# Performance work log

Measured on AMD Instinct MI355X. Metric: run time of the kernel, lower is better.

## Reference

```python
import jax, jax.numpy as jnp
import numpy as np

P_MINUS_1 = 1.0      # p=2 -> (p-1)
LCP_BETA = 32.0
LOG_ALPHA = float(np.log(2.0))  # alpha=2.0
KDIG = 8
N_HEAD = 16


def _rope(x, cos, sin):
    # x: (B,T,H,D), cos/sin: (T,D//2)
    d = x.shape[-1] // 2
    x1, x2 = x[..., :d], x[..., d:]
    c = cos[None, :, None, :]
    s = sin[None, :, None, :]
    return jnp.concatenate([x1 * c - x2 * s, x1 * s + x2 * c], axis=-1)


def _rms_norm(x, eps=1e-6):
    return x * jax.lax.rsqrt(jnp.mean(jnp.square(x), axis=-1, keepdims=True) + eps)


def setup_inputs() -> dict:
    key = jax.random.key(0)
    ks = jax.random.split(key, 9)
    B, T, C, H = 2, 512, 1024, N_HEAD
    D = C // H
    std = 0.02
    x = jax.random.normal(ks[0], (B, T, C), jnp.float32)
    cos = jax.random.uniform(ks[1], (T, D // 2), jnp.float32)
    sin = jax.random.uniform(ks[2], (T, D // 2), jnp.float32)
    Wq = jax.random.normal(ks[3], (C, C), jnp.float32) * std
    Wk = jax.random.normal(ks[4], (C, C), jnp.float32) * std
    Wv = jax.random.normal(ks[5], (C, C), jnp.float32) * std
    Wo = jax.random.normal(ks[6], (C, C), jnp.float32) * std
    # to_digits_* use flax default lecun_normal: std = 1/sqrt(fan_in)
    Wdq = jax.random.normal(ks[7], (D, KDIG), jnp.float32) / np.sqrt(D)
    Wdk = jax.random.normal(ks[8], (D, KDIG), jnp.float32) / np.sqrt(D)
    return {"x": x, "cos": cos, "sin": sin, "Wq": Wq, "Wk": Wk, "Wv": Wv,
            "Wo": Wo, "Wdq": Wdq, "Wdk": Wdk}


def _soft_lcp_depth(q_digits, k_digits):
    # q_digits: (B,H,Tq,K), k_digits: (B,H,Tk,K) -> (B,H,Tq,Tk)
    diff = jnp.abs(q_digits[:, :, :, None, :] - k_digits[:, :, None, :, :])
    match_prob = jnp.exp(-LCP_BETA * jnp.square(diff))
    prefix_prob = jnp.cumprod(match_prob, axis=-1)
    return jnp.sum(prefix_prob, axis=-1)


def reference(x, cos, sin, Wq, Wk, Wv, Wo, Wdq, Wdk):
    B, T, C = x.shape
    H = N_HEAD
    D = C // H
    q = (x @ Wq).reshape(B, T, H, D)
    k = (x @ Wk).reshape(B, T, H, D)
    v = (x @ Wv).reshape(B, T, H, D)
    q = _rms_norm(_rope(q, cos, sin))
    k = _rms_norm(_rope(k, cos, sin))
    q = jnp.transpose(q, (0, 2, 1, 3))  # (B,H,T,D)
    k = jnp.transpose(k, (0, 2, 1, 3))
    v = jnp.transpose(v, (0, 2, 1, 3))
    # causal keep mask (T,T), broadcast over (B,H)
    keep = jnp.tril(jnp.ones((T, T), dtype=bool))[None, None]
    q_digits = jax.nn.sigmoid((q @ Wdq).astype(jnp.float32)) * P_MINUS_1
    k_digits = jax.nn.sigmoid((k @ Wdk).astype(jnp.float32)) * P_MINUS_1
    lcp = _soft_lcp_depth(q_digits, k_digits)  # (B,H,T,T)
    weights = jnp.exp(lcp * LOG_ALPHA)
    weights = jnp.where(keep, weights, 0.0)
    denom = jnp.maximum(jnp.sum(weights, axis=-1, keepdims=True), 1e-9)
    attn = weights / denom
    y = jnp.einsum('bhqk,bhkd->bhqd', attn.astype(v.dtype), v)
    y = jnp.transpose(y, (0, 2, 1, 3)).reshape(B, T, C)
    return y @ Wo
```

## Files before the change

### kernel.cpp

```cpp
#include <hip/hip_runtime.h>

#define T_SEQ 512
#define CDIM  1024
#define NH    16
#define DH    64
#define BB    2
#define KD    8

#define BETA_LOG2E 46.16624131f
#define LOG2E      1.4426950408889634f

typedef unsigned short u16;
typedef __attribute__((ext_vector_type(8))) short bf16x8;
typedef __attribute__((ext_vector_type(4))) float f32x4;

__device__ inline u16 f2bf(float f) {
    unsigned int u = __builtin_bit_cast(unsigned int, f);
    unsigned int r = (u + 0x7fffu + ((u >> 16) & 1u)) >> 16;
    return (u16)r;
}
__device__ inline float bf2f(u16 v) {
    unsigned int u = ((unsigned int)v) << 16;
    return __builtin_bit_cast(float, u);
}

__device__ inline void gload_lds16(const void* g, void* l) {
    __builtin_amdgcn_global_load_lds(
        (const __attribute__((address_space(1))) void*)g,
        (__attribute__((address_space(3))) void*)l, 16, 0, 0);
}

__global__ __launch_bounds__(256)
void prep_kernel(const float* __restrict__ x,
                 const float* __restrict__ W0, const float* __restrict__ W1,
                 const float* __restrict__ W2, const float* __restrict__ W3,
                 u16* __restrict__ xb,
                 u16* __restrict__ T0, u16* __restrict__ T1,
                 u16* __restrict__ T2, u16* __restrict__ T3)
{
    const int tid = threadIdx.x;
    if (blockIdx.z == 4) {
        const int row = blockIdx.y * 32 + (tid >> 3);
        const int col = blockIdx.x * 32 + (tid & 7) * 4;
        float4 v = *(const float4*)&x[(size_t)row * CDIM + col];
        ushort4 o = { f2bf(v.x), f2bf(v.y), f2bf(v.z), f2bf(v.w) };
        *(ushort4*)&xb[(size_t)row * CDIM + col] = o;
        return;
    }
    __shared__ u16 tile[32][33];
    const float* W = (blockIdx.z == 0) ? W0 : (blockIdx.z == 1) ? W1
                   : (blockIdx.z == 2) ? W2 : W3;
    u16* Tt        = (blockIdx.z == 0) ? T0 : (blockIdx.z == 1) ? T1
                   : (blockIdx.z == 2) ? T2 : T3;
    const int k0 = blockIdx.y * 32, n0 = blockIdx.x * 32;
    const int r = tid >> 3, c4 = (tid & 7) * 4;

    float4 v = *(const float4*)&W[(size_t)(k0 + r) * CDIM + n0 + c4];
    tile[r][c4 + 0] = f2bf(v.x);
    tile[r][c4 + 1] = f2bf(v.y);
    tile[r][c4 + 2] = f2bf(v.z);
    tile[r][c4 + 3] = f2bf(v.w);
    __syncthreads();
    ushort4 o;
    o.x = tile[c4 + 0][r];
    o.y = tile[c4 + 1][r];
    o.z = tile[c4 + 2][r];
    o.w = tile[c4 + 3][r];
    *(ushort4*)&Tt[(size_t)(n0 + r) * CDIM + k0 + c4] = o;
}

__global__ __launch_bounds__(256)
void gemm_qkv_fused(const u16* __restrict__ A,
                    const u16* __restrict__ Bq, const u16* __restrict__ Bk,
                    const u16* __restrict__ Bv,
                    const float* __restrict__ cosp, const float* __restrict__ sinp,
                    const float* __restrict__ Wdq, const float* __restrict__ Wdk,
                    float* __restrict__ qdig, float* __restrict__ kdig,
                    u16* __restrict__ Vt)
{
    __shared__ __align__(16) char smem[64 * 65 * 4];
    u16* As = (u16*)smem;
    u16* Bs = As + 4096;
    float* Cf = (float*)smem;

    const int z = blockIdx.z;
    const u16* Bt = (z == 0) ? Bq : (z == 1) ? Bk : Bv;

    const int tid = threadIdx.x;
    const int l = tid & 63, w = tid >> 6;
    const int m0 = blockIdx.y * 64;
    const int h  = blockIdx.x;
    const int n0 = h * 64;
    const int wr = (w >> 1) * 32, wc = (w & 1) * 32;

    const int srow = l >> 3;
    const int sslot = (l & 7) ^ srow;

    f32x4 acc[2][2];
    #pragma unroll
    for (int i = 0; i < 2; ++i)
        #pragma unroll
        for (int j = 0; j < 2; ++j)
            acc[i][j] = (f32x4){0.f, 0.f, 0.f, 0.f};

    for (int k0 = 0; k0 < CDIM; k0 += 64) {
        __syncthreads();
        #pragma unroll
        for (int q = 0; q < 2; ++q) {
            const int row = w * 16 + q * 8 + srow;
            gload_lds16(A  + (size_t)(m0 + row) * CDIM + k0 + sslot * 8,
                        &As[(w * 16 + q * 8) * 64]);
            gload_lds16(Bt + (size_t)(n0 + row) * CDIM + k0 + sslot * 8,
                        &Bs[(w * 16 + q * 8) * 64]);
        }
        __syncthreads();

        bf16x8 af[2][2], bfr[2][2];
        #pragma unroll
        for (int i = 0; i < 2; ++i)
            #pragma unroll
            for (int kh = 0; kh < 2; ++kh) {
                const int ra = wr + i * 16 + (l & 15);
                const int sa = (kh * 4 + (l >> 4)) ^ (ra & 7);
                af[i][kh] = *(const bf16x8*)&As[ra * 64 + sa * 8];
                const int rb = wc + i * 16 + (l & 15);
                const int sb = (kh * 4 + (l >> 4)) ^ (rb & 7);
                bfr[i][kh] = *(const bf16x8*)&Bs[rb * 64 + sb * 8];
            }
        #pragma unroll
        for (int kh = 0; kh < 2; ++kh)
            #pragma unroll
            for (int i = 0; i < 2; ++i)
                #pragma unroll
                for (int j = 0; j < 2; ++j)
                    acc[i][j] = __builtin_amdgcn_mfma_f32_16x16x32_bf16(
                        af[i][kh], bfr[j][kh], acc[i][j], 0, 0, 0);
    }

    __syncthreads();

    if (z == 2) {
        #pragma unroll
        for (int i = 0; i < 2; ++i)
            #pragma unroll
            for (int j = 0; j < 2; ++j) {
                const int mm = wr + i * 16 + (l >> 4) * 4;
                const int dd = wc + j * 16 + (l & 15);
                #pragma unroll
                for (int r = 0; r < 4; ++r)
                    Cf[dd * 65 + mm + r] = acc[i][j][r];
            }
        __syncthreads();
        const int b = m0 >> 9, t0 = m0 & (T_SEQ - 1);
        u16* vbase = Vt + ((size_t)(b * NH + h) * 64) * T_SEQ;
        #pragma unroll
        for (int it = 0; it < 16; ++it) {
            const int d = it * 4 + w;
            vbase[(size_t)d * T_SEQ + t0 + l] = f2bf(Cf[d * 65 + l]);
        }
        return;
    }

    #pragma unroll
    for (int i = 0; i < 2; ++i)
        #pragma unroll
        for (int j = 0; j < 2; ++j) {
            const int mm = wr + i * 16 + (l >> 4) * 4;
            const int dd = wc + j * 16 + (l & 15);
            #pragma unroll
            for (int r = 0; r < 4; ++r)
                Cf[(mm + r) * 65 + dd] = acc[i][j][r];
        }

    const float* Wd = z ? Wdk : Wdq;
    float* dig = z ? kdig : qdig;

    const int dl = l & 15, rq = l >> 4;
    float wreg[4][8];
    #pragma unroll
    for (int d4 = 0; d4 < 4; ++d4) {
        *(float4*)&wreg[d4][0] = *(const float4*)&Wd[(dl + d4 * 16) * 8];
        *(float4*)&wreg[d4][4] = *(const float4*)&Wd[(dl + d4 * 16) * 8 + 4];
    }
    __syncthreads();

    for (int g = 0; g < 4; ++g) {
        const int m = w * 16 + g * 4 + rq;
        const int mg = m0 + m;
        const int b = mg >> 9, t = mg & (T_SEQ - 1);

        const float* cr = &Cf[m * 65];
        float r0 = cr[dl], r1 = cr[dl + 16], r2 = cr[dl + 32], r3 = cr[dl + 48];
        float c0 = cosp[t * 32 + dl], c1 = cosp[t * 32 + dl + 16];
        float s0 = sinp[t * 32 + dl], s1 = sinp[t * 32 + dl + 16];
        float v0 = r0 * c0 - r2 * s0;
        float v1 = r1 * c1 - r3 * s1;
        float v2 = r0 * s0 + r2 * c0;
        float v3 = r1 * s1 + r3 * c1;

        float ss = v0 * v0 + v1 * v1 + v2 * v2 + v3 * v3;
        #pragma unroll
        for (int off = 1; off < 16; off <<= 1) ss += __shfl_xor(ss, off);
        float sc = rsqrtf(ss * (1.0f / 64.0f) + 1e-6f);
        v0 *= sc; v1 *= sc; v2 *= sc; v3 *= sc;

        float zz[8];
        #pragma unroll
        for (int j = 0; j < 8; ++j)
            zz[j] = v0 * wreg[0][j] + v1 * wreg[1][j] + v2 * wreg[2][j] + v3 * wreg[3][j];
        #pragma unroll
        for (int j = 0; j < 8; ++j) {
            #pragma unroll
            for (int off = 1; off < 16; off <<= 1) zz[j] += __shfl_xor(zz[j], off);
        }
        float zsel = zz[0];
        #pragma unroll
        for (int j = 1; j < 8; ++j) zsel = (dl == j) ? zz[j] : zsel;
        if (dl < 8)
            dig[((size_t)(b * NH + h) * T_SEQ + t) * KD + dl] =
                1.0f / (1.0f + exp2f(-LOG2E * zsel));
    }
}

__global__ __launch_bounds__(256)
void attn_partial(const float* __restrict__ qdig, const float* __restrict__ kdig,
                  const u16* __restrict__ Vt,
                  u16* __restrict__ pacc, float* __restrict__ pdeng)
{
    __shared__ u16 Vs[4096];
    __shared__ u16 Ps[4096];
    __shared__ float qds[512];

    const int tid = threadIdx.x;
    const int w = tid >> 6, l = tid & 63;
    const int h = blockIdx.y, b = blockIdx.z;
    const int bh = b * NH + h;
    const size_t bhT = (size_t)bh * T_SEQ;

    int id = blockIdx.x, c = 0;
    while (id >= c + 1) { id -= (c + 1); ++c; }
    const int kt = id;
    const int k0 = kt * 64;

    const int srow = l >> 3, sslot = (l & 7) ^ srow;
    #pragma unroll
    for (int q2 = 0; q2 < 2; ++q2) {
        const int R0 = w * 16 + q2 * 8;
        gload_lds16(Vt + ((size_t)bh * 64 + R0 + srow) * T_SEQ + k0 + sslot * 8,
                    &Vs[R0 * 64]);
    }
    *(float2*)&qds[tid * 2] = *(const float2*)&qdig[(bhT + c * 64) * KD + tid * 2];

    float kd[8];
    {
        const float* kp = &kdig[(bhT + k0 + l) * KD];
        *(float4*)&kd[0] = *(const float4*)kp;
        *(float4*)&kd[4] = *(const float4*)(kp + 4);
    }
    __syncthreads();

    const bool diag = (kt == c);
    for (int qi = 0; qi < 16; ++qi) {
        const int qrow = w * 16 + qi;
        float qd[8];
        *(float4*)&qd[0] = *(const float4*)&qds[qrow * 8];
        *(float4*)&qd[4] = *(const float4*)&qds[qrow * 8 + 4];
        float cum = 1.f, lcp = 0.f;
        #pragma unroll
        for (int jj = 0; jj < 8; ++jj) {
            float d = qd[jj] - kd[jj];
            cum *= exp2f(-BETA_LOG2E * d * d);
            lcp += cum;
        }
        float wgt = exp2f(lcp);
        if (diag && l > qrow) wgt = 0.f;
        Ps[qrow * 64 + (((l >> 3) ^ (qi & 7)) << 3) + (l & 7)] = f2bf(wgt);
    }
    __syncthreads();

    const int wr = (w >> 1) * 32, wc = (w & 1) * 32;
    f32x4 acc[2][2], accd[2];
    #pragma unroll
    for (int i = 0; i < 2; ++i) {
        accd[i] = (f32x4){0.f, 0.f, 0.f, 0.f};
        #pragma unroll
        for (int j = 0; j < 2; ++j) acc[i][j] = (f32x4){0.f, 0.f, 0.f, 0.f};
    }
    bf16x8 ones;
    #pragma unroll
    for (int i = 0; i < 8; ++i) ones[i] = (short)0x3F80;

    #pragma unroll
    for (int kh = 0; kh < 2; ++kh) {
        bf16x8 af[2], bfr[2];
        #pragma unroll
        for (int i = 0; i < 2; ++i) {
            const int ra = wr + i * 16 + (l & 15);
            const int sa = (kh * 4 + (l >> 4)) ^ (ra & 7);
            af[i] = *(const bf16x8*)&Ps[ra * 64 + sa * 8];
            const int rb = wc + i * 16 + (l & 15);
            const int sb = (kh * 4 + (l >> 4)) ^ (rb & 7);
            bfr[i] = *(const bf16x8*)&Vs[rb * 64 + sb * 8];
        }
        #pragma unroll
        for (int i = 0; i < 2; ++i) {
            accd[i] = __builtin_amdgcn_mfma_f32_16x16x32_bf16(af[i], ones, accd[i], 0, 0, 0);
            #pragma unroll
            for (int j = 0; j < 2; ++j)
                acc[i][j] = __builtin_amdgcn_mfma_f32_16x16x32_bf16(
                    af[i], bfr[j], acc[i][j], 0, 0, 0);
        }
    }

    const int task = bh * 36 + blockIdx.x;
    u16* pa = pacc + (size_t)task * 4096;
    #pragma unroll
    for (int i = 0; i < 2; ++i) {
        const int row = wr + i * 16 + (l >> 4) * 4;
        #pragma unroll
        for (int j = 0; j < 2; ++j) {
            const int col = wc + j * 16 + (l & 15);
            #pragma unroll
            for (int r = 0; r < 4; ++r)
                pa[(size_t)(row + r) * 64 + col] = f2bf(acc[i][j][r]);
        }
        if ((l & 15) == 0) {
            #pragma unroll
            for (int r = 0; r < 4; ++r)
                pdeng[(size_t)task * 64 + row + r] = accd[i][r];
        }
    }
}

__global__ __launch_bounds__(256)
void attn_combine(const u16* __restrict__ pacc, const float* __restrict__ pdeng,
                  u16* __restrict__ y)
{
    const int c = blockIdx.x, h = blockIdx.y, b = blockIdx.z;
    const int tid = threadIdx.x;
    const int r = tid >> 2, dg = (tid & 3) * 16;
    const int base = (b * NH + h) * 36 + c * (c + 1) / 2;

    float acc[16] = {};
    float den = 0.f;
    for (int kt = 0; kt <= c; ++kt) {
        const u16* pa = pacc + (size_t)(base + kt) * 4096 + r * 64 + dg;
        ushort4 v0 = *(const ushort4*)(pa + 0);
        ushort4 v1 = *(const ushort4*)(pa + 4);
        ushort4 v2 = *(const ushort4*)(pa + 8);
        ushort4 v3 = *(const ushort4*)(pa + 12);
        acc[0]  += bf2f(v0.x); acc[1]  += bf2f(v0.y);
        acc[2]  += bf2f(v0.z); acc[3]  += bf2f(v0.w);
        acc[4]  += bf2f(v1.x); acc[5]  += bf2f(v1.y);
        acc[6]  += bf2f(v1.z); acc[7]  += bf2f(v1.w);
        acc[8]  += bf2f(v2.x); acc[9]  += bf2f(v2.y);
        acc[10] += bf2f(v2.z); acc[11] += bf2f(v2.w);
        acc[12] += bf2f(v3.x); acc[13] += bf2f(v3.y);
        acc[14] += bf2f(v3.z); acc[15] += bf2f(v3.w);
        den += pdeng[(size_t)(base + kt) * 64 + r];
    }
    float inv = 1.f / fmaxf(den, 1e-9f);

    u16* yr = y + ((size_t)(b * T_SEQ + c * 64 + r)) * CDIM + h * DH + dg;
    uint4 p0, p1;
    p0.x = f2bf(acc[0] * inv)  | ((unsigned)f2bf(acc[1] * inv)  << 16);
    p0.y = f2bf(acc[2] * inv)  | ((unsigned)f2bf(acc[3] * inv)  << 16);
    p0.z = f2bf(acc[4] * inv)  | ((unsigned)f2bf(acc[5] * inv)  << 16);
    p0.w = f2bf(acc[6] * inv)  | ((unsigned)f2bf(acc[7] * inv)  << 16);
    p1.x = f2bf(acc[8] * inv)  | ((unsigned)f2bf(acc[9] * inv)  << 16);
    p1.y = f2bf(acc[10] * inv) | ((unsigned)f2bf(acc[11] * inv) << 16);
    p1.z = f2bf(acc[12] * inv) | ((unsigned)f2bf(acc[13] * inv) << 16);
    p1.w = f2bf(acc[14] * inv) | ((unsigned)f2bf(acc[15] * inv) << 16);
    *(uint4*)(yr + 0) = p0;
    *(uint4*)(yr + 8) = p1;
}

__global__ __launch_bounds__(256)
void gemm_proj(const u16* __restrict__ A, const u16* __restrict__ Bt,
               float* __restrict__ C)
{
    __shared__ u16 As[32 * 64];
    __shared__ u16 Bs[64 * 64];

    const int tid = threadIdx.x;
    const int l = tid & 63, w = tid >> 6;
    const int m0 = blockIdx.y * 32, n0 = blockIdx.x * 64;
    const int wr = (w & 1) * 16, wc = (w >> 1) * 32;
    const int srow = l >> 3;
    const int sslot = (l & 7) ^ srow;

    f32x4 acc[2];
    acc[0] = (f32x4){0.f, 0.f, 0.f, 0.f};
    acc[1] = (f32x4){0.f, 0.f, 0.f, 0.f};

    for (int k0 = 0; k0 < CDIM; k0 += 64) {
        __syncthreads();
        {
            const int rowa = w * 8 + srow;
            gload_lds16(A + (size_t)(m0 + rowa) * CDIM + k0 + sslot * 8,
                        &As[(w * 8) * 64]);
        }
        #pragma unroll
        for (int q = 0; q < 2; ++q) {
            const int row = w * 16 + q * 8 + srow;
            gload_lds16(Bt + (size_t)(n0 + row) * CDIM + k0 + sslot * 8,
                        &Bs[(w * 16 + q * 8) * 64]);
        }
        __syncthreads();

        bf16x8 af[2], bfr[2][2];
        #pragma unroll
        for (int kh = 0; kh < 2; ++kh) {
            const int ra = wr + (l & 15);
            const int sa = (kh * 4 + (l >> 4)) ^ (ra & 7);
            af[kh] = *(const bf16x8*)&As[ra * 64 + sa * 8];
            #pragma unroll
            for (int j = 0; j < 2; ++j) {
                const int rb = wc + j * 16 + (l & 15);
                const int sb = (kh * 4 + (l >> 4)) ^ (rb & 7);
                bfr[j][kh] = *(const bf16x8*)&Bs[rb * 64 + sb * 8];
            }
        }
        #pragma unroll
        for (int kh = 0; kh < 2; ++kh)
            #pragma unroll
            for (int j = 0; j < 2; ++j)
                acc[j] = __builtin_amdgcn_mfma_f32_16x16x32_bf16(
                    af[kh], bfr[j][kh], acc[j], 0, 0, 0);
    }

    #pragma unroll
    for (int j = 0; j < 2; ++j) {
        const int row = m0 + wr + (l >> 4) * 4;
        const int col = n0 + wc + j * 16 + (l & 15);
        #pragma unroll
        for (int r = 0; r < 4; ++r)
            C[(size_t)(row + r) * CDIM + col] = acc[j][r];
    }
}

extern "C" void kernel_launch(void* const* d_in, const int* in_sizes, int n_in,
                              void* d_out, int out_size, void* d_ws, size_t ws_size,
                              hipStream_t stream)
{
    (void)in_sizes; (void)n_in; (void)out_size; (void)ws_size;
    const float* x    = (const float*)d_in[0];
    const float* cosp = (const float*)d_in[1];
    const float* sinp = (const float*)d_in[2];
    const float* Wq   = (const float*)d_in[3];
    const float* Wk   = (const float*)d_in[4];
    const float* Wv   = (const float*)d_in[5];
    const float* Wo   = (const float*)d_in[6];
    const float* Wdq  = (const float*)d_in[7];
    const float* Wdk  = (const float*)d_in[8];
    float* out = (float*)d_out;

    const int M = BB * T_SEQ;
    const size_t MC = (size_t)M * CDIM;
    char* p = (char*)d_ws;
    float* qdig = (float*)p; p += (size_t)M * NH * KD * 4;
    float* kdig = (float*)p; p += (size_t)M * NH * KD * 4;
    u16* xb   = (u16*)p; p += MC * 2;
    u16* wqt  = (u16*)p; p += MC * 2;
    u16* wkt  = (u16*)p; p += MC * 2;
    u16* wvt  = (u16*)p; p += MC * 2;
    u16* wot  = (u16*)p; p += MC * 2;
    u16* Vt   = (u16*)p; p += MC * 2;
    u16* ybuf = (u16*)p; p += MC * 2;
    u16* pacc = (u16*)p; p += (size_t)1152 * 4096 * 2;
    float* pdeng = (float*)p; p += (size_t)1152 * 64 * 4;

    dim3 blk(256);
    prep_kernel<<<dim3(32, 32, 5), blk, 0, stream>>>(
        x, Wq, Wk, Wv, Wo, xb, wqt, wkt, wvt, wot);
    gemm_qkv_fused<<<dim3(16, 16, 3), blk, 0, stream>>>(
        xb, wqt, wkt, wvt, cosp, sinp, Wdq, Wdk, qdig, kdig, Vt);
    attn_partial<<<dim3(36, NH, BB), blk, 0, stream>>>(
        qdig, kdig, Vt, pacc, pdeng);
    attn_combine<<<dim3(8, NH, BB), blk, 0, stream>>>(pacc, pdeng, ybuf);
    gemm_proj<<<dim3(16, 32), blk, 0, stream>>>(ybuf, wot, out);
}
```

Measured before the change: 59.41 us.

## Deepen GEMM K tiles, remap blocks across XCDs, simplify LCP exp chain

```diff
diff --git a/kernel.cpp b/kernel.cpp
--- a/kernel.cpp
+++ b/kernel.cpp
@@ -78,23 +78,23 @@
                     float* __restrict__ qdig, float* __restrict__ kdig,
                     u16* __restrict__ Vt)
 {
-    __shared__ __align__(16) char smem[64 * 65 * 4];
+    __shared__ __align__(16) char smem[32768];
     u16* As = (u16*)smem;
-    u16* Bs = As + 4096;
+    u16* Bs = As + 8192;
     float* Cf = (float*)smem;
 
-    const int z = blockIdx.z;
+    const int wg = (blockIdx.x & 7) * 96 + (blockIdx.x >> 3);
+    const int z = wg >> 8;
+    const int rem = wg & 255;
+    const int h = rem & 15;
+    const int m0 = (rem >> 4) * 64;
+    const int n0 = h * 64;
+
     const u16* Bt = (z == 0) ? Bq : (z == 1) ? Bk : Bv;
 
     const int tid = threadIdx.x;
     const int l = tid & 63, w = tid >> 6;
-    const int m0 = blockIdx.y * 64;
-    const int h  = blockIdx.x;
-    const int n0 = h * 64;
     const int wr = (w >> 1) * 32, wc = (w & 1) * 32;
-
-    const int srow = l >> 3;
-    const int sslot = (l & 7) ^ srow;
 
     f32x4 acc[2][2];
     #pragma unroll
@@ -103,38 +103,38 @@
         for (int j = 0; j < 2; ++j)
             acc[i][j] = (f32x4){0.f, 0.f, 0.f, 0.f};
 
-    for (int k0 = 0; k0 < CDIM; k0 += 64) {
+    for (int k0 = 0; k0 < CDIM; k0 += 128) {
         __syncthreads();
         #pragma unroll
-        for (int q = 0; q < 2; ++q) {
-            const int row = w * 16 + q * 8 + srow;
-            gload_lds16(A  + (size_t)(m0 + row) * CDIM + k0 + sslot * 8,
-                        &As[(w * 16 + q * 8) * 64]);
-            gload_lds16(Bt + (size_t)(n0 + row) * CDIM + k0 + sslot * 8,
-                        &Bs[(w * 16 + q * 8) * 64]);
+        for (int q = 0; q < 4; ++q) {
+            const int row = w * 16 + q * 4 + (l >> 4);
+            const int slot = (l & 15) ^ (row & 15);
+            gload_lds16(A  + (size_t)(m0 + row) * CDIM + k0 + slot * 8,
+                        &As[(w * 16 + q * 4) * 128]);
+            gload_lds16(Bt + (size_t)(n0 + row) * CDIM + k0 + slot * 8,
+                        &Bs[(w * 16 + q * 4) * 128]);
         }
         __syncthreads();
 
-        bf16x8 af[2][2], bfr[2][2];
-        #pragma unroll
-        for (int i = 0; i < 2; ++i)
-            #pragma unroll
-            for (int kh = 0; kh < 2; ++kh) {
+        #pragma unroll
+        for (int kh = 0; kh < 4; ++kh) {
+            bf16x8 af[2], bfr[2];
+            #pragma unroll
+            for (int i = 0; i < 2; ++i) {
                 const int ra = wr + i * 16 + (l & 15);
-                const int sa = (kh * 4 + (l >> 4)) ^ (ra & 7);
-                af[i][kh] = *(const bf16x8*)&As[ra * 64 + sa * 8];
+                const int sa = (kh * 4 + (l >> 4)) ^ (ra & 15);
+                af[i] = *(const bf16x8*)&As[ra * 128 + sa * 8];
                 const int rb = wc + i * 16 + (l & 15);
-                const int sb = (kh * 4 + (l >> 4)) ^ (rb & 7);
-                bfr[i][kh] = *(const bf16x8*)&Bs[rb * 64 + sb * 8];
+                const int sb = (kh * 4 + (l >> 4)) ^ (rb & 15);
+                bfr[i] = *(const bf16x8*)&Bs[rb * 128 + sb * 8];
             }
-        #pragma unroll
-        for (int kh = 0; kh < 2; ++kh)
             #pragma unroll
             for (int i = 0; i < 2; ++i)
                 #pragma unroll
                 for (int j = 0; j < 2; ++j)
                     acc[i][j] = __builtin_amdgcn_mfma_f32_16x16x32_bf16(
-                        af[i][kh], bfr[j][kh], acc[i][j], 0, 0, 0);
+                        af[i], bfr[j], acc[i][j], 0, 0, 0);
+        }
     }
 
     __syncthreads();
@@ -233,11 +233,13 @@
 
     const int tid = threadIdx.x;
     const int w = tid >> 6, l = tid & 63;
-    const int h = blockIdx.y, b = blockIdx.z;
-    const int bh = b * NH + h;
+
+    const int wg = (blockIdx.x & 7) * 144 + (blockIdx.x >> 3);
+    const int tile = wg % 36;
+    const int bh = wg / 36;
     const size_t bhT = (size_t)bh * T_SEQ;
 
-    int id = blockIdx.x, c = 0;
+    int id = tile, c = 0;
     while (id >= c + 1) { id -= (c + 1); ++c; }
     const int kt = id;
     const int k0 = kt * 64;
@@ -265,12 +267,12 @@
         float qd[8];
         *(float4*)&qd[0] = *(const float4*)&qds[qrow * 8];
         *(float4*)&qd[4] = *(const float4*)&qds[qrow * 8 + 4];
-        float cum = 1.f, lcp = 0.f;
+        float S = 0.f, lcp = 0.f;
         #pragma unroll
         for (int jj = 0; jj < 8; ++jj) {
             float d = qd[jj] - kd[jj];
-            cum *= exp2f(-BETA_LOG2E * d * d);
-            lcp += cum;
+            S += d * d;
+            lcp += exp2f(-BETA_LOG2E * S);
         }
         float wgt = exp2f(lcp);
         if (diag && l > qrow) wgt = 0.f;
@@ -312,7 +314,7 @@
         }
     }
 
-    const int task = bh * 36 + blockIdx.x;
+    const int task = bh * 36 + tile;
     u16* pa = pacc + (size_t)task * 4096;
     #pragma unroll
     for (int i = 0; i < 2; ++i) {
@@ -336,97 +338,86 @@
 void attn_combine(const u16* __restrict__ pacc, const float* __restrict__ pdeng,
                   u16* __restrict__ y)
 {
-    const int c = blockIdx.x, h = blockIdx.y, b = blockIdx.z;
+    const int c = blockIdx.x >> 1, half = blockIdx.x & 1;
+    const int h = blockIdx.y, b = blockIdx.z;
     const int tid = threadIdx.x;
-    const int r = tid >> 2, dg = (tid & 3) * 16;
+    const int r = tid >> 2, cg = (tid & 3) * 8 + half * 32;
     const int base = (b * NH + h) * 36 + c * (c + 1) / 2;
 
-    float acc[16] = {};
+    float acc[8] = {};
     float den = 0.f;
     for (int kt = 0; kt <= c; ++kt) {
-        const u16* pa = pacc + (size_t)(base + kt) * 4096 + r * 64 + dg;
+        const u16* pa = pacc + (size_t)(base + kt) * 4096 + r * 64 + cg;
         ushort4 v0 = *(const ushort4*)(pa + 0);
         ushort4 v1 = *(const ushort4*)(pa + 4);
-        ushort4 v2 = *(const ushort4*)(pa + 8);
-        ushort4 v3 = *(const ushort4*)(pa + 12);
-        acc[0]  += bf2f(v0.x); acc[1]  += bf2f(v0.y);
-        acc[2]  += bf2f(v0.z); acc[3]  += bf2f(v0.w);
-        acc[4]  += bf2f(v1.x); acc[5]  += bf2f(v1.y);
-        acc[6]  += bf2f(v1.z); acc[7]  += bf2f(v1.w);
-        acc[8]  += bf2f(v2.x); acc[9]  += bf2f(v2.y);
-        acc[10] += bf2f(v2.z); acc[11] += bf2f(v2.w);
-        acc[12] += bf2f(v3.x); acc[13] += bf2f(v3.y);
-        acc[14] += bf2f(v3.z); acc[15] += bf2f(v3.w);
+        acc[0] += bf2f(v0.x); acc[1] += bf2f(v0.y);
+        acc[2] += bf2f(v0.z); acc[3] += bf2f(v0.w);
+        acc[4] += bf2f(v1.x); acc[5] += bf2f(v1.y);
+        acc[6] += bf2f(v1.z); acc[7] += bf2f(v1.w);
         den += pdeng[(size_t)(base + kt) * 64 + r];
     }
     float inv = 1.f / fmaxf(den, 1e-9f);
 
-    u16* yr = y + ((size_t)(b * T_SEQ + c * 64 + r)) * CDIM + h * DH + dg;
-    uint4 p0, p1;
-    p0.x = f2bf(acc[0] * inv)  | ((unsigned)f2bf(acc[1] * inv)  << 16);
-    p0.y = f2bf(acc[2] * inv)  | ((unsigned)f2bf(acc[3] * inv)  << 16);
-    p0.z = f2bf(acc[4] * inv)  | ((unsigned)f2bf(acc[5] * inv)  << 16);
-    p0.w = f2bf(acc[6] * inv)  | ((unsigned)f2bf(acc[7] * inv)  << 16);
-    p1.x = f2bf(acc[8] * inv)  | ((unsigned)f2bf(acc[9] * inv)  << 16);
-    p1.y = f2bf(acc[10] * inv) | ((unsigned)f2bf(acc[11] * inv) << 16);
-    p1.z = f2bf(acc[12] * inv) | ((unsigned)f2bf(acc[13] * inv) << 16);
-    p1.w = f2bf(acc[14] * inv) | ((unsigned)f2bf(acc[15] * inv) << 16);
-    *(uint4*)(yr + 0) = p0;
-    *(uint4*)(yr + 8) = p1;
+    u16* yr = y + ((size_t)(b * T_SEQ + c * 64 + r)) * CDIM + h * DH + cg;
+    uint4 p;
+    p.x = f2bf(acc[0] * inv) | ((unsigned)f2bf(acc[1] * inv) << 16);
+    p.y = f2bf(acc[2] * inv) | ((unsigned)f2bf(acc[3] * inv) << 16);
+    p.z = f2bf(acc[4] * inv) | ((unsigned)f2bf(acc[5] * inv) << 16);
+    p.w = f2bf(acc[6] * inv) | ((unsigned)f2bf(acc[7] * inv) << 16);
+    *(uint4*)yr = p;
 }
 
 __global__ __launch_bounds__(256)
 void gemm_proj(const u16* __restrict__ A, const u16* __restrict__ Bt,
                float* __restrict__ C)
 {
-    __shared__ u16 As[32 * 64];
-    __shared__ u16 Bs[64 * 64];
+    __shared__ u16 As[32 * 128];
+    __shared__ u16 Bs[64 * 128];
+
+    const int wg = (blockIdx.x & 7) * 64 + (blockIdx.x >> 3);
+    const int n0 = (wg & 15) * 64;
+    const int m0 = (wg >> 4) * 32;
 
     const int tid = threadIdx.x;
     const int l = tid & 63, w = tid >> 6;
-    const int m0 = blockIdx.y * 32, n0 = blockIdx.x * 64;
     const int wr = (w & 1) * 16, wc = (w >> 1) * 32;
-    const int srow = l >> 3;
-    const int sslot = (l & 7) ^ srow;
 
     f32x4 acc[2];
     acc[0] = (f32x4){0.f, 0.f, 0.f, 0.f};
     acc[1] = (f32x4){0.f, 0.f, 0.f, 0.f};
 
-    for (int k0 = 0; k0 < CDIM; k0 += 64) {
+    for (int k0 = 0; k0 < CDIM; k0 += 128) {
         __syncthreads();
-        {
-            const int rowa = w * 8 + srow;
-            gload_lds16(A + (size_t)(m0 + rowa) * CDIM + k0 + sslot * 8,
-                        &As[(w * 8) * 64]);
-        }
         #pragma unroll
         for (int q = 0; q < 2; ++q) {
-            const int row = w * 16 + q * 8 + srow;
-            gload_lds16(Bt + (size_t)(n0 + row) * CDIM + k0 + sslot * 8,
-                        &Bs[(w * 16 + q * 8) * 64]);
+            const int rowa = w * 8 + q * 4 + (l >> 4);
+            const int slota = (l & 15) ^ (rowa & 15);
+            gload_lds16(A + (size_t)(m0 + rowa) * CDIM + k0 + slota * 8,
+                        &As[(w * 8 + q * 4) * 128]);
+        }
+        #pragma unroll
+        for (int q = 0; q < 4; ++q) {
+            const int row = w * 16 + q * 4 + (l >> 4);
+            const int slot = (l & 15) ^ (row & 15);
+            gload_lds16(Bt + (size_t)(n0 + row) * CDIM + k0 + slot * 8,
+                        &Bs[(w * 16 + q * 4) * 128]);
         }
         __syncthreads();
 
-        bf16x8 af[2], bfr[2][2];
-        #pragma unroll
-        for (int kh = 0; kh < 2; ++kh) {
+        #pragma unroll
+        for (int kh = 0; kh < 4; ++kh) {
             const int ra = wr + (l & 15);
-            const int sa = (kh * 4 + (l >> 4)) ^ (ra & 7);
-            af[kh] = *(const bf16x8*)&As[ra * 64 + sa * 8];
+            const int sa = (kh * 4 + (l >> 4)) ^ (ra & 15);
+            bf16x8 af = *(const bf16x8*)&As[ra * 128 + sa * 8];
             #pragma unroll
             for (int j = 0; j < 2; ++j) {
                 const int rb = wc + j * 16 + (l & 15);
-                const int sb = (kh * 4 + (l >> 4)) ^ (rb & 7);
-                bfr[j][kh] = *(const bf16x8*)&Bs[rb * 64 + sb * 8];
+                const int sb = (kh * 4 + (l >> 4)) ^ (rb & 15);
+                bf16x8 bfr = *(const bf16x8*)&Bs[rb * 128 + sb * 8];
+                acc[j] = __builtin_amdgcn_mfma_f32_16x16x32_bf16(
+                    af, bfr, acc[j], 0, 0, 0);
             }
         }
-        #pragma unroll
-        for (int kh = 0; kh < 2; ++kh)
-            #pragma unroll
-            for (int j = 0; j < 2; ++j)
-                acc[j] = __builtin_amdgcn_mfma_f32_16x16x32_bf16(
-                    af[kh], bfr[j][kh], acc[j], 0, 0, 0);
     }
 
     #pragma unroll
@@ -473,10 +464,10 @@
     dim3 blk(256);
     prep_kernel<<<dim3(32, 32, 5), blk, 0, stream>>>(
         x, Wq, Wk, Wv, Wo, xb, wqt, wkt, wvt, wot);
-    gemm_qkv_fused<<<dim3(16, 16, 3), blk, 0, stream>>>(
+    gemm_qkv_fused<<<dim3(768), blk, 0, stream>>>(
         xb, wqt, wkt, wvt, cosp, sinp, Wdq, Wdk, qdig, kdig, Vt);
-    attn_partial<<<dim3(36, NH, BB), blk, 0, stream>>>(
+    attn_partial<<<dim3(1152), blk, 0, stream>>>(
         qdig, kdig, Vt, pacc, pdeng);
-    attn_combine<<<dim3(8, NH, BB), blk, 0, stream>>>(pacc, pdeng, ybuf);
-    gemm_proj<<<dim3(16, 32), blk, 0, stream>>>(ybuf, wot, out);
-}
+    attn_combine<<<dim3(16, NH, BB), blk, 0, stream>>>(pacc, pdeng, ybuf);
+    gemm_proj<<<dim3(512), blk, 0, stream>>>(ybuf, wot, out);
+}
```

New measurement: 58.72 us. About the same (-1.1%).
